# Kernel optimization log

Measured on AMD Instinct MI355X. Metric: run time of the kernel, lower is better.

The kernel has to match this reference:

```python
import jax, jax.numpy as jnp
import numpy as np


def setup_inputs() -> dict:
    key = jax.random.key(0)
    kq, kk, kv = jax.random.split(key, 3)
    B, H, S, D = 2, 16, 2048, 64
    q = jax.random.normal(kq, (B, H, S, D), dtype=jnp.float32)
    k = jax.random.normal(kk, (B, H, S, D), dtype=jnp.float32)
    v = jax.random.normal(kv, (B, H, S, D), dtype=jnp.float32)
    return {"q": q, "k": k, "v": v}


def reference(q, k, v):
    # q,k,v: [B,H,S,D]
    d_tensor = q.shape[-1]
    scale = 1.0 / jnp.sqrt(jnp.asarray(d_tensor, dtype=q.dtype))
    # score: [B,H,S,S] -- full unfused score matrix, as in the original
    score = jnp.einsum("bhsd,bhtd->bhst", q, k) * scale
    score = jax.nn.softmax(score, axis=-1)
    out = jnp.einsum("bhst,bhtd->bhsd", score, v)
    return (out, score)
```

## Files before the change

### kernel.cpp

```cpp
#include <hip/hip_runtime.h>
#include <hip/hip_bf16.h>

#define S_LEN 2048
#define D_DIM 64
#define NWAVE 4
#define NTHR  256
#define QW    32
#define QB    (QW * NWAVE)
#define NBH   32
#define CHK   128
#define NCHK  (S_LEN / CHK)
#define NE    ((size_t)NBH * S_LEN * D_DIM)

typedef __attribute__((ext_vector_type(4)))  float f32x4;
typedef __attribute__((ext_vector_type(16))) float f32x16;
typedef __attribute__((ext_vector_type(8)))  short s16x8;
typedef __attribute__((ext_vector_type(2)))  int   i32x2;

union FU { float f; unsigned int u; };
union PU { unsigned int u[4]; s16x8 v; };

__device__ __forceinline__ float bf2f(unsigned short h){
    FU x; x.u = ((unsigned int)h) << 16; return x.f;
}
__device__ __forceinline__ unsigned short f2bf(float f){
    __hip_bfloat16 h = __float2bfloat16(f);
    return __builtin_bit_cast(unsigned short, h);
}
__device__ __forceinline__ s16x8 cvt8(const float* p, float s){
    f32x4 a = *(const f32x4*)p, b = *(const f32x4*)(p + 4);
    s16x8 f;
    f[0]=(short)f2bf(a[0]*s); f[1]=(short)f2bf(a[1]*s); f[2]=(short)f2bf(a[2]*s); f[3]=(short)f2bf(a[3]*s);
    f[4]=(short)f2bf(b[0]*s); f[5]=(short)f2bf(b[1]*s); f[6]=(short)f2bf(b[2]*s); f[7]=(short)f2bf(b[3]*s);
    return f;
}

typedef __attribute__((address_space(3))) unsigned short lds_us;
typedef __attribute__((address_space(1))) const unsigned short glb_us;
__device__ __forceinline__ void gl16(const unsigned short* g, unsigned short* l){
    __builtin_amdgcn_global_load_lds((glb_us*)g, (lds_us*)l, 16, 0, 0);
}

__device__ __forceinline__ void plswap(unsigned int& a, unsigned int& b){
#if __has_builtin(__builtin_amdgcn_permlane32_swap)
    i32x2 r = __builtin_amdgcn_permlane32_swap((int)a, (int)b, false, false);
    a = (unsigned int)r[0];
    b = (unsigned int)r[1];
#else
    const int ad = ((threadIdx.x & 63) ^ 32) * 4;
    const int ax = __builtin_amdgcn_ds_bpermute(ad, (int)a);
    const int bx = __builtin_amdgcn_ds_bpermute(ad, (int)b);
    const bool hi = (threadIdx.x & 32) != 0;
    unsigned int na = hi ? (unsigned int)bx : a;
    unsigned int nb = hi ? b : (unsigned int)ax;
    a = na; b = nb;
#endif
}

__global__ __launch_bounds__(256)
void cvt_bf16_kernel(const float* __restrict__ src, unsigned short* __restrict__ dst,
                     float scale, int n8)
{
    int i = blockIdx.x * 256 + threadIdx.x;
    if (i >= n8) return;
    *(s16x8*)(dst + (size_t)i * 8) = cvt8(src + (size_t)i * 8, scale);
}

__global__ __launch_bounds__(256)
void transpose_v_kernel(const float* __restrict__ V, unsigned short* __restrict__ Vt)
{
    __shared__ float tile[64][65];
    const int bh = blockIdx.y;
    const int s0 = blockIdx.x * 64;
    const int t  = threadIdx.x;
    const int r  = t >> 2;
    const int cs = (t & 3) * 16;

    const float* src = V + ((size_t)bh * S_LEN + s0 + r) * D_DIM + cs;
    #pragma unroll
    for (int j = 0; j < 16; j += 4){
        f32x4 v = *(const f32x4*)(src + j);
        tile[r][cs + j + 0] = v[0]; tile[r][cs + j + 1] = v[1];
        tile[r][cs + j + 2] = v[2]; tile[r][cs + j + 3] = v[3];
    }
    __syncthreads();
    s16x8 o0, o1;
    #pragma unroll
    for (int j = 0; j < 8; ++j)  o0[j] = (short)f2bf(tile[cs + j][r]);
    #pragma unroll
    for (int j = 0; j < 8; ++j)  o1[j] = (short)f2bf(tile[cs + 8 + j][r]);
    unsigned short* dst = Vt + ((size_t)bh * D_DIM + r) * S_LEN + s0 + cs;
    *(s16x8*)dst       = o0;
    *(s16x8*)(dst + 8) = o1;
}

__global__ __launch_bounds__(NTHR, 2)
void sdpa_main(const unsigned short* __restrict__ Qb,
               const unsigned short* __restrict__ Kb,
               const unsigned short* __restrict__ Vt,
               float* __restrict__ Out, float* __restrict__ Score)
{
    __shared__ unsigned short kbuf[2][CHK * D_DIM];
    __shared__ unsigned short vbuf[2][D_DIM * CHK];

    const int id  = blockIdx.x;
    const int j   = id >> 3;
    const int bh  = (id & 7) * 4 + (j >> 4);
    const int qt  = j & 15;

    const int tid = threadIdx.x;
    const int w   = tid >> 6;
    const int l   = tid & 63;
    const int h   = l >> 5;
    const int q32 = l & 31;

    const unsigned short* Kbh = Kb + (size_t)bh * S_LEN * D_DIM;
    const unsigned short* Vbh = Vt + (size_t)bh * D_DIM * S_LEN;
    const int qrow = qt * QB + w * QW;

    auto stageK = [&](int c, int b){
        #pragma unroll
        for (int i = 0; i < 4; ++i){
            const int idx = i*64 + l;
            const int row = w*32 + (idx >> 3);
            const int us  = (idx & 7) ^ (row & 7);
            gl16(Kbh + ((size_t)(c*CHK + row)) * D_DIM + us*8,
                 &kbuf[b][(w*256 + i*64) * 8]);
        }
    };
    auto stageV = [&](int c, int b){
        #pragma unroll
        for (int i = 0; i < 4; ++i){
            const int idx = i*64 + l;
            const int row = w*16 + (idx >> 4);
            const int us  = (idx & 15) ^ (row & 15);
            gl16(Vbh + (size_t)row * S_LEN + c*CHK + us*8,
                 &vbuf[b][(w*256 + i*64) * 8]);
        }
    };

    s16x8 qB[4];
    {
        const unsigned short* qp = Qb + ((size_t)bh * S_LEN + qrow + q32) * D_DIM + h*8;
        #pragma unroll
        for (int s = 0; s < 4; ++s) qB[s] = *(const s16x8*)(qp + s*16);
    }

    float lsum = 0.f;
    stageK(0, 0);
    __syncthreads();
    for (int c = 0; c < NCHK; ++c){
        if (c + 1 < NCHK) stageK(c + 1, (c + 1) & 1);
        const unsigned short* kb = &kbuf[c & 1][0];
        #pragma unroll
        for (int kt = 0; kt < 4; ++kt){
            const int row = kt*32 + q32;
            f32x16 acc = {0.f,0.f,0.f,0.f,0.f,0.f,0.f,0.f,0.f,0.f,0.f,0.f,0.f,0.f,0.f,0.f};
            #pragma unroll
            for (int s = 0; s < 4; ++s){
                const int su = (2*s + h) ^ (row & 7);
                const s16x8 a = *(const s16x8*)(kb + row*D_DIM + su*8);
                acc = __builtin_amdgcn_mfma_f32_32x32x16_bf16(a, qB[s], acc, 0, 0, 0);
            }
            #pragma unroll
            for (int r = 0; r < 16; ++r)
                lsum += __expf(fminf(acc[r], 60.f));
        }
        __syncthreads();
    }
    lsum += __shfl_xor(lsum, 32, 64);
    const float invl = 1.0f / lsum;

    float invreg[16];
    #pragma unroll
    for (int r = 0; r < 16; ++r){
        const int qa = (r & 3) + 8*(r >> 2);
        invreg[r] = __shfl(invl, qa + 4*h, 64);
    }

    f32x16 oacc[2];
    oacc[0] = (f32x16){0.f,0.f,0.f,0.f,0.f,0.f,0.f,0.f,0.f,0.f,0.f,0.f,0.f,0.f,0.f,0.f};
    oacc[1] = oacc[0];

    stageK(0, 0);
    stageV(0, 0);
    __syncthreads();

    float* sbase = Score + ((size_t)bh * S_LEN + qrow + 4*h) * S_LEN + q32;

    for (int c = 0; c < NCHK; ++c){
        if (c + 1 < NCHK){ stageK(c + 1, (c + 1) & 1); stageV(c + 1, (c + 1) & 1); }
        const unsigned short* kb = &kbuf[c & 1][0];
        const unsigned short* vb = &vbuf[c & 1][0];

        #pragma unroll
        for (int kt = 0; kt < 4; ++kt){
            const int row = kt*32 + q32;
            f32x16 acc  = {0.f,0.f,0.f,0.f,0.f,0.f,0.f,0.f,0.f,0.f,0.f,0.f,0.f,0.f,0.f,0.f};
            f32x16 acc2 = acc;
            #pragma unroll
            for (int s = 0; s < 4; ++s){
                const int su = (2*s + h) ^ (row & 7);
                const s16x8 a = *(const s16x8*)(kb + row*D_DIM + su*8);
                acc  = __builtin_amdgcn_mfma_f32_32x32x16_bf16(a, qB[s], acc,  0, 0, 0);
                acc2 = __builtin_amdgcn_mfma_f32_32x32x16_bf16(qB[s], a, acc2, 0, 0, 0);
            }

            #pragma unroll
            for (int r = 0; r < 16; ++r){
                const int qa = (r & 3) + 8*(r >> 2);
                const float e = __expf(fminf(acc2[r], 60.f)) * invreg[r];
                __builtin_nontemporal_store(e, sbase + (size_t)qa * S_LEN + c*CHK + kt*32);
            }

            float e[16];
            #pragma unroll
            for (int r = 0; r < 16; ++r) e[r] = __expf(fminf(acc[r], 60.f));

            unsigned int pk[8];
            #pragma unroll
            for (int p = 0; p < 8; ++p)
                pk[p] = (unsigned int)f2bf(e[2*p]) | ((unsigned int)f2bf(e[2*p+1]) << 16);

            plswap(pk[0], pk[2]);
            plswap(pk[1], pk[3]);
            plswap(pk[4], pk[6]);
            plswap(pk[5], pk[7]);
            PU p0, p1;
            p0.u[0] = pk[0]; p0.u[1] = pk[1]; p0.u[2] = pk[2]; p0.u[3] = pk[3];
            p1.u[0] = pk[4]; p1.u[1] = pk[5]; p1.u[2] = pk[6]; p1.u[3] = pk[7];

            #pragma unroll
            for (int dt = 0; dt < 2; ++dt){
                const int d   = dt*32 + q32;
                const int su0 = (4*kt + h)     ^ (d & 15);
                const int su1 = (4*kt + 2 + h) ^ (d & 15);
                const s16x8 v0 = *(const s16x8*)(vb + d*CHK + su0*8);
                const s16x8 v1 = *(const s16x8*)(vb + d*CHK + su1*8);
                oacc[dt] = __builtin_amdgcn_mfma_f32_32x32x16_bf16(v0, p0.v, oacc[dt], 0, 0, 0);
                oacc[dt] = __builtin_amdgcn_mfma_f32_32x32x16_bf16(v1, p1.v, oacc[dt], 0, 0, 0);
            }
        }
        __syncthreads();
    }

    float* orow = Out + ((size_t)bh * S_LEN + qrow + q32) * D_DIM;
    #pragma unroll
    for (int dt = 0; dt < 2; ++dt){
        #pragma unroll
        for (int g = 0; g < 4; ++g){
            f32x4 o = { oacc[dt][4*g+0]*invl, oacc[dt][4*g+1]*invl,
                        oacc[dt][4*g+2]*invl, oacc[dt][4*g+3]*invl };
            *(f32x4*)(orow + dt*32 + 4*h + 8*g) = o;
        }
    }
}

__global__ __launch_bounds__(256)
void sdpa_naive(const float* __restrict__ Q, const float* __restrict__ K,
                const float* __restrict__ V, float* __restrict__ Out,
                float* __restrict__ Score)
{
    const int bh = blockIdx.y;
    const int qi = blockIdx.x;
    __shared__ float srow[S_LEN];
    __shared__ float qs[D_DIM];
    __shared__ float red[256];
    const int t = threadIdx.x;
    const float* qp = Q + ((size_t)bh * S_LEN + qi) * D_DIM;
    if (t < D_DIM) qs[t] = qp[t] * 0.125f;
    __syncthreads();
    float m = -1e30f;
    for (int k = t; k < S_LEN; k += 256){
        const float* kp = K + ((size_t)bh * S_LEN + k) * D_DIM;
        float s = 0.f;
        for (int d = 0; d < D_DIM; ++d) s += qs[d] * kp[d];
        srow[k] = s;
        m = fmaxf(m, s);
    }
    red[t] = m; __syncthreads();
    for (int o = 128; o; o >>= 1){ if (t < o) red[t] = fmaxf(red[t], red[t + o]); __syncthreads(); }
    m = red[0]; __syncthreads();
    float sum = 0.f;
    for (int k = t; k < S_LEN; k += 256){ float e = __expf(srow[k] - m); srow[k] = e; sum += e; }
    red[t] = sum; __syncthreads();
    for (int o = 128; o; o >>= 1){ if (t < o) red[t] += red[t + o]; __syncthreads(); }
    const float inv = 1.0f / red[0];
    float* sout = Score + ((size_t)bh * S_LEN + qi) * S_LEN;
    for (int k = t; k < S_LEN; k += 256) sout[k] = srow[k] * inv;
    if (t < D_DIM){
        float acc = 0.f;
        for (int k = 0; k < S_LEN; ++k) acc += srow[k] * V[((size_t)bh * S_LEN + k) * D_DIM + t];
        Out[((size_t)bh * S_LEN + qi) * D_DIM + t] = acc * inv;
    }
}

extern "C" void kernel_launch(void* const* d_in, const int* in_sizes, int n_in,
                              void* d_out, int out_size, void* d_ws, size_t ws_size,
                              hipStream_t stream)
{
    const float* q = (const float*)d_in[0];
    const float* k = (const float*)d_in[1];
    const float* v = (const float*)d_in[2];
    float* out   = (float*)d_out;
    float* score = out + NE;

    if (ws_size >= 3 * NE * sizeof(unsigned short)){
        unsigned short* Qb = (unsigned short*)d_ws;
        unsigned short* Kb = Qb + NE;
        unsigned short* Vt = Kb + NE;
        const int n8 = (int)(NE / 8);
        cvt_bf16_kernel<<<(n8 + 255) / 256, 256, 0, stream>>>(q, Qb, 0.125f, n8);
        cvt_bf16_kernel<<<(n8 + 255) / 256, 256, 0, stream>>>(k, Kb, 1.0f, n8);
        transpose_v_kernel<<<dim3(S_LEN / 64, NBH), 256, 0, stream>>>(v, Vt);
        sdpa_main<<<(S_LEN / QB) * NBH, NTHR, 0, stream>>>(Qb, Kb, Vt, out, score);
    } else {
        sdpa_naive<<<dim3(S_LEN, NBH), 256, 0, stream>>>(q, k, v, out, score);
    }
}
```

Before: 180.5 us.

## Split row-sum pass into separate kernel and use smaller 64-row tiles

```diff
diff --git a/kernel.cpp b/kernel.cpp
--- a/kernel.cpp
+++ b/kernel.cpp
@@ -3,14 +3,16 @@
 
 #define S_LEN 2048
 #define D_DIM 64
-#define NWAVE 4
-#define NTHR  256
-#define QW    32
-#define QB    (QW * NWAVE)
 #define NBH   32
-#define CHK   128
-#define NCHK  (S_LEN / CHK)
 #define NE    ((size_t)NBH * S_LEN * D_DIM)
+
+#define QB2   64
+#define CHK2  64
+#define NCHK2 (S_LEN / CHK2)
+
+#define QBF   128
+#define CHKF  128
+#define NCHKF (S_LEN / CHKF)
 
 typedef __attribute__((ext_vector_type(4)))  float f32x4;
 typedef __attribute__((ext_vector_type(16))) float f32x16;
@@ -94,50 +96,24 @@
     *(s16x8*)(dst + 8) = o1;
 }
 
-__global__ __launch_bounds__(NTHR, 2)
-void sdpa_main(const unsigned short* __restrict__ Qb,
-               const unsigned short* __restrict__ Kb,
-               const unsigned short* __restrict__ Vt,
-               float* __restrict__ Out, float* __restrict__ Score)
-{
-    __shared__ unsigned short kbuf[2][CHK * D_DIM];
-    __shared__ unsigned short vbuf[2][D_DIM * CHK];
-
+__global__ __launch_bounds__(128, 4)
+void pass1_lsum(const unsigned short* __restrict__ Qb,
+                const unsigned short* __restrict__ Kb,
+                float* __restrict__ invl)
+{
     const int id  = blockIdx.x;
     const int j   = id >> 3;
-    const int bh  = (id & 7) * 4 + (j >> 4);
-    const int qt  = j & 15;
+    const int bh  = (id & 7) * 4 + (j >> 5);
+    const int qt  = j & 31;
 
     const int tid = threadIdx.x;
     const int w   = tid >> 6;
     const int l   = tid & 63;
     const int h   = l >> 5;
     const int q32 = l & 31;
+    const int qrow = qt * QB2 + w * 32;
 
     const unsigned short* Kbh = Kb + (size_t)bh * S_LEN * D_DIM;
-    const unsigned short* Vbh = Vt + (size_t)bh * D_DIM * S_LEN;
-    const int qrow = qt * QB + w * QW;
-
-    auto stageK = [&](int c, int b){
-        #pragma unroll
-        for (int i = 0; i < 4; ++i){
-            const int idx = i*64 + l;
-            const int row = w*32 + (idx >> 3);
-            const int us  = (idx & 7) ^ (row & 7);
-            gl16(Kbh + ((size_t)(c*CHK + row)) * D_DIM + us*8,
-                 &kbuf[b][(w*256 + i*64) * 8]);
-        }
-    };
-    auto stageV = [&](int c, int b){
-        #pragma unroll
-        for (int i = 0; i < 4; ++i){
-            const int idx = i*64 + l;
-            const int row = w*16 + (idx >> 4);
-            const int us  = (idx & 15) ^ (row & 15);
-            gl16(Vbh + (size_t)row * S_LEN + c*CHK + us*8,
-                 &vbuf[b][(w*256 + i*64) * 8]);
-        }
-    };
 
     s16x8 qB[4];
     {
@@ -147,35 +123,82 @@
     }
 
     float lsum = 0.f;
-    stageK(0, 0);
-    __syncthreads();
-    for (int c = 0; c < NCHK; ++c){
-        if (c + 1 < NCHK) stageK(c + 1, (c + 1) & 1);
-        const unsigned short* kb = &kbuf[c & 1][0];
-        #pragma unroll
-        for (int kt = 0; kt < 4; ++kt){
-            const int row = kt*32 + q32;
-            f32x16 acc = {0.f,0.f,0.f,0.f,0.f,0.f,0.f,0.f,0.f,0.f,0.f,0.f,0.f,0.f,0.f,0.f};
-            #pragma unroll
-            for (int s = 0; s < 4; ++s){
-                const int su = (2*s + h) ^ (row & 7);
-                const s16x8 a = *(const s16x8*)(kb + row*D_DIM + su*8);
-                acc = __builtin_amdgcn_mfma_f32_32x32x16_bf16(a, qB[s], acc, 0, 0, 0);
-            }
-            #pragma unroll
-            for (int r = 0; r < 16; ++r)
-                lsum += __expf(fminf(acc[r], 60.f));
-        }
-        __syncthreads();
+    #pragma unroll 2
+    for (int kt = 0; kt < S_LEN / 32; ++kt){
+        const unsigned short* kr = Kbh + (size_t)(kt*32 + q32) * D_DIM + h*8;
+        f32x16 acc = {0.f,0.f,0.f,0.f,0.f,0.f,0.f,0.f,0.f,0.f,0.f,0.f,0.f,0.f,0.f,0.f};
+        #pragma unroll
+        for (int s = 0; s < 4; ++s){
+            const s16x8 a = *(const s16x8*)(kr + s*16);
+            acc = __builtin_amdgcn_mfma_f32_32x32x16_bf16(a, qB[s], acc, 0, 0, 0);
+        }
+        #pragma unroll
+        for (int r = 0; r < 16; ++r)
+            lsum += __expf(fminf(acc[r], 60.f));
     }
     lsum += __shfl_xor(lsum, 32, 64);
-    const float invl = 1.0f / lsum;
-
+    if (l < 32) invl[(size_t)bh * S_LEN + qrow + l] = 1.0f / lsum;
+}
+
+__global__ __launch_bounds__(128, 2)
+void sdpa_split(const unsigned short* __restrict__ Qb,
+                const unsigned short* __restrict__ Kb,
+                const unsigned short* __restrict__ Vt,
+                const float* __restrict__ invl,
+                float* __restrict__ Out, float* __restrict__ Score)
+{
+    __shared__ unsigned short kbuf[2][CHK2 * D_DIM];
+    __shared__ unsigned short vbuf[2][D_DIM * CHK2];
+
+    const int id  = blockIdx.x;
+    const int j   = id >> 3;
+    const int bh  = (id & 7) * 4 + (j >> 5);
+    const int qt  = j & 31;
+
+    const int tid = threadIdx.x;
+    const int w   = tid >> 6;
+    const int l   = tid & 63;
+    const int h   = l >> 5;
+    const int q32 = l & 31;
+    const int qrow = qt * QB2 + w * 32;
+
+    const unsigned short* Kbh = Kb + (size_t)bh * S_LEN * D_DIM;
+    const unsigned short* Vbh = Vt + (size_t)bh * D_DIM * S_LEN;
+
+    auto stageK = [&](int c, int b){
+        #pragma unroll
+        for (int i = 0; i < 4; ++i){
+            const int slot = i*128 + w*64 + l;
+            const int row  = slot >> 3;
+            const int us   = (slot & 7) ^ (row & 7);
+            gl16(Kbh + ((size_t)(c*CHK2 + row)) * D_DIM + us*8,
+                 &kbuf[b][(i*128 + w*64) * 8]);
+        }
+    };
+    auto stageV = [&](int c, int b){
+        #pragma unroll
+        for (int i = 0; i < 4; ++i){
+            const int slot = i*128 + w*64 + l;
+            const int row  = slot >> 3;
+            const int us   = (slot & 7) ^ (row & 7);
+            gl16(Vbh + (size_t)row * S_LEN + c*CHK2 + us*8,
+                 &vbuf[b][(i*128 + w*64) * 8]);
+        }
+    };
+
+    s16x8 qB[4];
+    {
+        const unsigned short* qp = Qb + ((size_t)bh * S_LEN + qrow + q32) * D_DIM + h*8;
+        #pragma unroll
+        for (int s = 0; s < 4; ++s) qB[s] = *(const s16x8*)(qp + s*16);
+    }
+
+    const float invl_lane = invl[(size_t)bh * S_LEN + qrow + q32];
     float invreg[16];
     #pragma unroll
     for (int r = 0; r < 16; ++r){
         const int qa = (r & 3) + 8*(r >> 2);
-        invreg[r] = __shfl(invl, qa + 4*h, 64);
+        invreg[r] = __shfl(invl_lane, qa + 4*h, 64);
     }
 
     f32x16 oacc[2];
@@ -188,13 +211,13 @@
 
     float* sbase = Score + ((size_t)bh * S_LEN + qrow + 4*h) * S_LEN + q32;
 
-    for (int c = 0; c < NCHK; ++c){
-        if (c + 1 < NCHK){ stageK(c + 1, (c + 1) & 1); stageV(c + 1, (c + 1) & 1); }
+    for (int c = 0; c < NCHK2; ++c){
+        if (c + 1 < NCHK2){ stageK(c + 1, (c + 1) & 1); stageV(c + 1, (c + 1) & 1); }
         const unsigned short* kb = &kbuf[c & 1][0];
         const unsigned short* vb = &vbuf[c & 1][0];
 
         #pragma unroll
-        for (int kt = 0; kt < 4; ++kt){
+        for (int kt = 0; kt < 2; ++kt){
             const int row = kt*32 + q32;
             f32x16 acc  = {0.f,0.f,0.f,0.f,0.f,0.f,0.f,0.f,0.f,0.f,0.f,0.f,0.f,0.f,0.f,0.f};
             f32x16 acc2 = acc;
@@ -210,7 +233,7 @@
             for (int r = 0; r < 16; ++r){
                 const int qa = (r & 3) + 8*(r >> 2);
                 const float e = __expf(fminf(acc2[r], 60.f)) * invreg[r];
-                __builtin_nontemporal_store(e, sbase + (size_t)qa * S_LEN + c*CHK + kt*32);
+                __builtin_nontemporal_store(e, sbase + (size_t)qa * S_LEN + c*CHK2 + kt*32);
             }
 
             float e[16];
@@ -233,10 +256,167 @@
             #pragma unroll
             for (int dt = 0; dt < 2; ++dt){
                 const int d   = dt*32 + q32;
+                const int su0 = (kt*4 + h)     ^ (d & 7);
+                const int su1 = (kt*4 + 2 + h) ^ (d & 7);
+                const s16x8 v0 = *(const s16x8*)(vb + d*CHK2 + su0*8);
+                const s16x8 v1 = *(const s16x8*)(vb + d*CHK2 + su1*8);
+                oacc[dt] = __builtin_amdgcn_mfma_f32_32x32x16_bf16(v0, p0.v, oacc[dt], 0, 0, 0);
+                oacc[dt] = __builtin_amdgcn_mfma_f32_32x32x16_bf16(v1, p1.v, oacc[dt], 0, 0, 0);
+            }
+        }
+        __syncthreads();
+    }
+
+    float* orow = Out + ((size_t)bh * S_LEN + qrow + q32) * D_DIM;
+    #pragma unroll
+    for (int dt = 0; dt < 2; ++dt){
+        #pragma unroll
+        for (int g = 0; g < 4; ++g){
+            f32x4 o = { oacc[dt][4*g+0]*invl_lane, oacc[dt][4*g+1]*invl_lane,
+                        oacc[dt][4*g+2]*invl_lane, oacc[dt][4*g+3]*invl_lane };
+            *(f32x4*)(orow + dt*32 + 4*h + 8*g) = o;
+        }
+    }
+}
+
+__global__ __launch_bounds__(256, 2)
+void sdpa_fused(const unsigned short* __restrict__ Qb,
+                const unsigned short* __restrict__ Kb,
+                const unsigned short* __restrict__ Vt,
+                float* __restrict__ Out, float* __restrict__ Score)
+{
+    __shared__ unsigned short kbuf[2][CHKF * D_DIM];
+    __shared__ unsigned short vbuf[2][D_DIM * CHKF];
+
+    const int id  = blockIdx.x;
+    const int j   = id >> 3;
+    const int bh  = (id & 7) * 4 + (j >> 4);
+    const int qt  = j & 15;
+
+    const int tid = threadIdx.x;
+    const int w   = tid >> 6;
+    const int l   = tid & 63;
+    const int h   = l >> 5;
+    const int q32 = l & 31;
+
+    const unsigned short* Kbh = Kb + (size_t)bh * S_LEN * D_DIM;
+    const unsigned short* Vbh = Vt + (size_t)bh * D_DIM * S_LEN;
+    const int qrow = qt * QBF + w * 32;
+
+    auto stageK = [&](int c, int b){
+        #pragma unroll
+        for (int i = 0; i < 4; ++i){
+            const int idx = i*64 + l;
+            const int row = w*32 + (idx >> 3);
+            const int us  = (idx & 7) ^ (row & 7);
+            gl16(Kbh + ((size_t)(c*CHKF + row)) * D_DIM + us*8,
+                 &kbuf[b][(w*256 + i*64) * 8]);
+        }
+    };
+    auto stageV = [&](int c, int b){
+        #pragma unroll
+        for (int i = 0; i < 4; ++i){
+            const int idx = i*64 + l;
+            const int row = w*16 + (idx >> 4);
+            const int us  = (idx & 15) ^ (row & 15);
+            gl16(Vbh + (size_t)row * S_LEN + c*CHKF + us*8,
+                 &vbuf[b][(w*256 + i*64) * 8]);
+        }
+    };
+
+    s16x8 qB[4];
+    {
+        const unsigned short* qp = Qb + ((size_t)bh * S_LEN + qrow + q32) * D_DIM + h*8;
+        #pragma unroll
+        for (int s = 0; s < 4; ++s) qB[s] = *(const s16x8*)(qp + s*16);
+    }
+
+    float lsum = 0.f;
+    stageK(0, 0);
+    __syncthreads();
+    for (int c = 0; c < NCHKF; ++c){
+        if (c + 1 < NCHKF) stageK(c + 1, (c + 1) & 1);
+        const unsigned short* kb = &kbuf[c & 1][0];
+        #pragma unroll
+        for (int kt = 0; kt < 4; ++kt){
+            const int row = kt*32 + q32;
+            f32x16 acc = {0.f,0.f,0.f,0.f,0.f,0.f,0.f,0.f,0.f,0.f,0.f,0.f,0.f,0.f,0.f,0.f};
+            #pragma unroll
+            for (int s = 0; s < 4; ++s){
+                const int su = (2*s + h) ^ (row & 7);
+                const s16x8 a = *(const s16x8*)(kb + row*D_DIM + su*8);
+                acc = __builtin_amdgcn_mfma_f32_32x32x16_bf16(a, qB[s], acc, 0, 0, 0);
+            }
+            #pragma unroll
+            for (int r = 0; r < 16; ++r)
+                lsum += __expf(fminf(acc[r], 60.f));
+        }
+        __syncthreads();
+    }
+    lsum += __shfl_xor(lsum, 32, 64);
+    const float invl = 1.0f / lsum;
+
+    float invreg[16];
+    #pragma unroll
+    for (int r = 0; r < 16; ++r){
+        const int qa = (r & 3) + 8*(r >> 2);
+        invreg[r] = __shfl(invl, qa + 4*h, 64);
+    }
+
+    f32x16 oacc[2];
+    oacc[0] = (f32x16){0.f,0.f,0.f,0.f,0.f,0.f,0.f,0.f,0.f,0.f,0.f,0.f,0.f,0.f,0.f,0.f};
+    oacc[1] = oacc[0];
+
+    stageK(0, 0);
+    stageV(0, 0);
+    __syncthreads();
+
+    float* sbase = Score + ((size_t)bh * S_LEN + qrow + 4*h) * S_LEN + q32;
+
+    for (int c = 0; c < NCHKF; ++c){
+        if (c + 1 < NCHKF){ stageK(c + 1, (c + 1) & 1); stageV(c + 1, (c + 1) & 1); }
+        const unsigned short* kb = &kbuf[c & 1][0];
+        const unsigned short* vb = &vbuf[c & 1][0];
+
+        #pragma unroll
+        for (int kt = 0; kt < 4; ++kt){
+            const int row = kt*32 + q32;
+            f32x16 acc  = {0.f,0.f,0.f,0.f,0.f,0.f,0.f,0.f,0.f,0.f,0.f,0.f,0.f,0.f,0.f,0.f};
+            f32x16 acc2 = acc;
+            #pragma unroll
+            for (int s = 0; s < 4; ++s){
+                const int su = (2*s + h) ^ (row & 7);
+                const s16x8 a = *(const s16x8*)(kb + row*D_DIM + su*8);
+                acc  = __builtin_amdgcn_mfma_f32_32x32x16_bf16(a, qB[s], acc,  0, 0, 0);
+                acc2 = __builtin_amdgcn_mfma_f32_32x32x16_bf16(qB[s], a, acc2, 0, 0, 0);
+            }
+            #pragma unroll
+            for (int r = 0; r < 16; ++r){
+                const int qa = (r & 3) + 8*(r >> 2);
+                const float e = __expf(fminf(acc2[r], 60.f)) * invreg[r];
+                __builtin_nontemporal_store(e, sbase + (size_t)qa * S_LEN + c*CHKF + kt*32);
+            }
+            float e[16];
+            #pragma unroll
+            for (int r = 0; r < 16; ++r) e[r] = __expf(fminf(acc[r], 60.f));
+            unsigned int pk[8];
+            #pragma unroll
+            for (int p = 0; p < 8; ++p)
+                pk[p] = (unsigned int)f2bf(e[2*p]) | ((unsigned int)f2bf(e[2*p+1]) << 16);
+            plswap(pk[0], pk[2]);
+            plswap(pk[1], pk[3]);
+            plswap(pk[4], pk[6]);
+            plswap(pk[5], pk[7]);
+            PU p0, p1;
+            p0.u[0] = pk[0]; p0.u[1] = pk[1]; p0.u[2] = pk[2]; p0.u[3] = pk[3];
+            p1.u[0] = pk[4]; p1.u[1] = pk[5]; p1.u[2] = pk[6]; p1.u[3] = pk[7];
+            #pragma unroll
+            for (int dt = 0; dt < 2; ++dt){
+                const int d   = dt*32 + q32;
                 const int su0 = (4*kt + h)     ^ (d & 15);
                 const int su1 = (4*kt + 2 + h) ^ (d & 15);
-                const s16x8 v0 = *(const s16x8*)(vb + d*CHK + su0*8);
-                const s16x8 v1 = *(const s16x8*)(vb + d*CHK + su1*8);
+                const s16x8 v0 = *(const s16x8*)(vb + d*CHKF + su0*8);
+                const s16x8 v1 = *(const s16x8*)(vb + d*CHKF + su1*8);
                 oacc[dt] = __builtin_amdgcn_mfma_f32_32x32x16_bf16(v0, p0.v, oacc[dt], 0, 0, 0);
                 oacc[dt] = __builtin_amdgcn_mfma_f32_32x32x16_bf16(v1, p1.v, oacc[dt], 0, 0, 0);
             }
@@ -305,7 +485,21 @@
     float* out   = (float*)d_out;
     float* score = out + NE;
 
-    if (ws_size >= 3 * NE * sizeof(unsigned short)){
+    const size_t need_bf16 = 3 * NE * sizeof(unsigned short);
+    const size_t need_full = need_bf16 + (size_t)NBH * S_LEN * sizeof(float);
+
+    if (ws_size >= need_full){
+        unsigned short* Qb = (unsigned short*)d_ws;
+        unsigned short* Kb = Qb + NE;
+        unsigned short* Vt = Kb + NE;
+        float* invl = (float*)(Vt + NE);
+        const int n8 = (int)(NE / 8);
+        cvt_bf16_kernel<<<(n8 + 255) / 256, 256, 0, stream>>>(q, Qb, 0.125f, n8);
+        cvt_bf16_kernel<<<(n8 + 255) / 256, 256, 0, stream>>>(k, Kb, 1.0f, n8);
+        transpose_v_kernel<<<dim3(S_LEN / 64, NBH), 256, 0, stream>>>(v, Vt);
+        pass1_lsum<<<(S_LEN / QB2) * NBH, 128, 0, stream>>>(Qb, Kb, invl);
+        sdpa_split<<<(S_LEN / QB2) * NBH, 128, 0, stream>>>(Qb, Kb, Vt, invl, out, score);
+    } else if (ws_size >= need_bf16){
         unsigned short* Qb = (unsigned short*)d_ws;
         unsigned short* Kb = Qb + NE;
         unsigned short* Vt = Kb + NE;
@@ -313,7 +507,7 @@
         cvt_bf16_kernel<<<(n8 + 255) / 256, 256, 0, stream>>>(q, Qb, 0.125f, n8);
         cvt_bf16_kernel<<<(n8 + 255) / 256, 256, 0, stream>>>(k, Kb, 1.0f, n8);
         transpose_v_kernel<<<dim3(S_LEN / 64, NBH), 256, 0, stream>>>(v, Vt);
-        sdpa_main<<<(S_LEN / QB) * NBH, NTHR, 0, stream>>>(Qb, Kb, Vt, out, score);
+        sdpa_fused<<<(S_LEN / QBF) * NBH, 256, 0, stream>>>(Qb, Kb, Vt, out, score);
     } else {
         sdpa_naive<<<dim3(S_LEN, NBH), 256, 0, stream>>>(q, k, v, out, score);
     }
```

Result: slower. 225.2 us (+24.8%).

## Drop LDS staging and load K/V fragments directly from global memory

Applied to the files above, without the earlier changes.

```diff
diff --git a/kernel.cpp b/kernel.cpp
--- a/kernel.cpp
+++ b/kernel.cpp
@@ -3,14 +3,9 @@
 
 #define S_LEN 2048
 #define D_DIM 64
-#define NWAVE 4
-#define NTHR  256
-#define QW    32
-#define QB    (QW * NWAVE)
 #define NBH   32
-#define CHK   128
-#define NCHK  (S_LEN / CHK)
 #define NE    ((size_t)NBH * S_LEN * D_DIM)
+#define NKT   (S_LEN / 32)
 
 typedef __attribute__((ext_vector_type(4)))  float f32x4;
 typedef __attribute__((ext_vector_type(16))) float f32x16;
@@ -33,12 +28,6 @@
     f[0]=(short)f2bf(a[0]*s); f[1]=(short)f2bf(a[1]*s); f[2]=(short)f2bf(a[2]*s); f[3]=(short)f2bf(a[3]*s);
     f[4]=(short)f2bf(b[0]*s); f[5]=(short)f2bf(b[1]*s); f[6]=(short)f2bf(b[2]*s); f[7]=(short)f2bf(b[3]*s);
     return f;
-}
-
-typedef __attribute__((address_space(3))) unsigned short lds_us;
-typedef __attribute__((address_space(1))) const unsigned short glb_us;
-__device__ __forceinline__ void gl16(const unsigned short* g, unsigned short* l){
-    __builtin_amdgcn_global_load_lds((glb_us*)g, (lds_us*)l, 16, 0, 0);
 }
 
 __device__ __forceinline__ void plswap(unsigned int& a, unsigned int& b){
@@ -94,15 +83,12 @@
     *(s16x8*)(dst + 8) = o1;
 }
 
-__global__ __launch_bounds__(NTHR, 2)
-void sdpa_main(const unsigned short* __restrict__ Qb,
-               const unsigned short* __restrict__ Kb,
-               const unsigned short* __restrict__ Vt,
-               float* __restrict__ Out, float* __restrict__ Score)
-{
-    __shared__ unsigned short kbuf[2][CHK * D_DIM];
-    __shared__ unsigned short vbuf[2][D_DIM * CHK];
-
+__global__ __launch_bounds__(256, 4)
+void sdpa_nolds(const unsigned short* __restrict__ Qb,
+                const unsigned short* __restrict__ Kb,
+                const unsigned short* __restrict__ Vt,
+                float* __restrict__ Out, float* __restrict__ Score)
+{
     const int id  = blockIdx.x;
     const int j   = id >> 3;
     const int bh  = (id & 7) * 4 + (j >> 4);
@@ -113,31 +99,10 @@
     const int l   = tid & 63;
     const int h   = l >> 5;
     const int q32 = l & 31;
+    const int qrow = qt * 128 + w * 32;
 
     const unsigned short* Kbh = Kb + (size_t)bh * S_LEN * D_DIM;
     const unsigned short* Vbh = Vt + (size_t)bh * D_DIM * S_LEN;
-    const int qrow = qt * QB + w * QW;
-
-    auto stageK = [&](int c, int b){
-        #pragma unroll
-        for (int i = 0; i < 4; ++i){
-            const int idx = i*64 + l;
-            const int row = w*32 + (idx >> 3);
-            const int us  = (idx & 7) ^ (row & 7);
-            gl16(Kbh + ((size_t)(c*CHK + row)) * D_DIM + us*8,
-                 &kbuf[b][(w*256 + i*64) * 8]);
-        }
-    };
-    auto stageV = [&](int c, int b){
-        #pragma unroll
-        for (int i = 0; i < 4; ++i){
-            const int idx = i*64 + l;
-            const int row = w*16 + (idx >> 4);
-            const int us  = (idx & 15) ^ (row & 15);
-            gl16(Vbh + (size_t)row * S_LEN + c*CHK + us*8,
-                 &vbuf[b][(w*256 + i*64) * 8]);
-        }
-    };
 
     s16x8 qB[4];
     {
@@ -146,27 +111,21 @@
         for (int s = 0; s < 4; ++s) qB[s] = *(const s16x8*)(qp + s*16);
     }
 
+    const unsigned short* kbase = Kbh + (size_t)q32 * D_DIM + h*8;
+
     float lsum = 0.f;
-    stageK(0, 0);
-    __syncthreads();
-    for (int c = 0; c < NCHK; ++c){
-        if (c + 1 < NCHK) stageK(c + 1, (c + 1) & 1);
-        const unsigned short* kb = &kbuf[c & 1][0];
-        #pragma unroll
-        for (int kt = 0; kt < 4; ++kt){
-            const int row = kt*32 + q32;
-            f32x16 acc = {0.f,0.f,0.f,0.f,0.f,0.f,0.f,0.f,0.f,0.f,0.f,0.f,0.f,0.f,0.f,0.f};
-            #pragma unroll
-            for (int s = 0; s < 4; ++s){
-                const int su = (2*s + h) ^ (row & 7);
-                const s16x8 a = *(const s16x8*)(kb + row*D_DIM + su*8);
-                acc = __builtin_amdgcn_mfma_f32_32x32x16_bf16(a, qB[s], acc, 0, 0, 0);
-            }
-            #pragma unroll
-            for (int r = 0; r < 16; ++r)
-                lsum += __expf(fminf(acc[r], 60.f));
-        }
-        __syncthreads();
+    #pragma unroll 2
+    for (int kt = 0; kt < NKT; ++kt){
+        const unsigned short* kr = kbase + (size_t)kt * 32 * D_DIM;
+        f32x16 acc = {0.f,0.f,0.f,0.f,0.f,0.f,0.f,0.f,0.f,0.f,0.f,0.f,0.f,0.f,0.f,0.f};
+        #pragma unroll
+        for (int s = 0; s < 4; ++s){
+            const s16x8 a = *(const s16x8*)(kr + s*16);
+            acc = __builtin_amdgcn_mfma_f32_32x32x16_bf16(a, qB[s], acc, 0, 0, 0);
+        }
+        #pragma unroll
+        for (int r = 0; r < 16; ++r)
+            lsum += __expf(fminf(acc[r], 60.f));
     }
     lsum += __shfl_xor(lsum, 32, 64);
     const float invl = 1.0f / lsum;
@@ -182,66 +141,55 @@
     oacc[0] = (f32x16){0.f,0.f,0.f,0.f,0.f,0.f,0.f,0.f,0.f,0.f,0.f,0.f,0.f,0.f,0.f,0.f};
     oacc[1] = oacc[0];
 
-    stageK(0, 0);
-    stageV(0, 0);
-    __syncthreads();
-
     float* sbase = Score + ((size_t)bh * S_LEN + qrow + 4*h) * S_LEN + q32;
 
-    for (int c = 0; c < NCHK; ++c){
-        if (c + 1 < NCHK){ stageK(c + 1, (c + 1) & 1); stageV(c + 1, (c + 1) & 1); }
-        const unsigned short* kb = &kbuf[c & 1][0];
-        const unsigned short* vb = &vbuf[c & 1][0];
-
-        #pragma unroll
-        for (int kt = 0; kt < 4; ++kt){
-            const int row = kt*32 + q32;
-            f32x16 acc  = {0.f,0.f,0.f,0.f,0.f,0.f,0.f,0.f,0.f,0.f,0.f,0.f,0.f,0.f,0.f,0.f};
-            f32x16 acc2 = acc;
-            #pragma unroll
-            for (int s = 0; s < 4; ++s){
-                const int su = (2*s + h) ^ (row & 7);
-                const s16x8 a = *(const s16x8*)(kb + row*D_DIM + su*8);
-                acc  = __builtin_amdgcn_mfma_f32_32x32x16_bf16(a, qB[s], acc,  0, 0, 0);
-                acc2 = __builtin_amdgcn_mfma_f32_32x32x16_bf16(qB[s], a, acc2, 0, 0, 0);
-            }
-
-            #pragma unroll
-            for (int r = 0; r < 16; ++r){
-                const int qa = (r & 3) + 8*(r >> 2);
-                const float e = __expf(fminf(acc2[r], 60.f)) * invreg[r];
-                __builtin_nontemporal_store(e, sbase + (size_t)qa * S_LEN + c*CHK + kt*32);
-            }
-
-            float e[16];
-            #pragma unroll
-            for (int r = 0; r < 16; ++r) e[r] = __expf(fminf(acc[r], 60.f));
-
-            unsigned int pk[8];
-            #pragma unroll
-            for (int p = 0; p < 8; ++p)
-                pk[p] = (unsigned int)f2bf(e[2*p]) | ((unsigned int)f2bf(e[2*p+1]) << 16);
-
-            plswap(pk[0], pk[2]);
-            plswap(pk[1], pk[3]);
-            plswap(pk[4], pk[6]);
-            plswap(pk[5], pk[7]);
-            PU p0, p1;
-            p0.u[0] = pk[0]; p0.u[1] = pk[1]; p0.u[2] = pk[2]; p0.u[3] = pk[3];
-            p1.u[0] = pk[4]; p1.u[1] = pk[5]; p1.u[2] = pk[6]; p1.u[3] = pk[7];
-
-            #pragma unroll
-            for (int dt = 0; dt < 2; ++dt){
-                const int d   = dt*32 + q32;
-                const int su0 = (4*kt + h)     ^ (d & 15);
-                const int su1 = (4*kt + 2 + h) ^ (d & 15);
-                const s16x8 v0 = *(const s16x8*)(vb + d*CHK + su0*8);
-                const s16x8 v1 = *(const s16x8*)(vb + d*CHK + su1*8);
-                oacc[dt] = __builtin_amdgcn_mfma_f32_32x32x16_bf16(v0, p0.v, oacc[dt], 0, 0, 0);
-                oacc[dt] = __builtin_amdgcn_mfma_f32_32x32x16_bf16(v1, p1.v, oacc[dt], 0, 0, 0);
-            }
-        }
-        __syncthreads();
+    for (int kt = 0; kt < NKT; ++kt){
+        const unsigned short* kr = kbase + (size_t)kt * 32 * D_DIM;
+        s16x8 kf[4];
+        #pragma unroll
+        for (int s = 0; s < 4; ++s) kf[s] = *(const s16x8*)(kr + s*16);
+
+        f32x16 acc2 = {0.f,0.f,0.f,0.f,0.f,0.f,0.f,0.f,0.f,0.f,0.f,0.f,0.f,0.f,0.f,0.f};
+        #pragma unroll
+        for (int s = 0; s < 4; ++s)
+            acc2 = __builtin_amdgcn_mfma_f32_32x32x16_bf16(qB[s], kf[s], acc2, 0, 0, 0);
+        #pragma unroll
+        for (int r = 0; r < 16; ++r){
+            const int qa = (r & 3) + 8*(r >> 2);
+            const float e = __expf(fminf(acc2[r], 60.f)) * invreg[r];
+            __builtin_nontemporal_store(e, sbase + (size_t)qa * S_LEN + kt*32);
+        }
+
+        f32x16 acc = {0.f,0.f,0.f,0.f,0.f,0.f,0.f,0.f,0.f,0.f,0.f,0.f,0.f,0.f,0.f,0.f};
+        #pragma unroll
+        for (int s = 0; s < 4; ++s)
+            acc = __builtin_amdgcn_mfma_f32_32x32x16_bf16(kf[s], qB[s], acc, 0, 0, 0);
+
+        float e[16];
+        #pragma unroll
+        for (int r = 0; r < 16; ++r) e[r] = __expf(fminf(acc[r], 60.f));
+
+        unsigned int pk[8];
+        #pragma unroll
+        for (int p = 0; p < 8; ++p)
+            pk[p] = (unsigned int)f2bf(e[2*p]) | ((unsigned int)f2bf(e[2*p+1]) << 16);
+
+        plswap(pk[0], pk[2]);
+        plswap(pk[1], pk[3]);
+        plswap(pk[4], pk[6]);
+        plswap(pk[5], pk[7]);
+        PU p0, p1;
+        p0.u[0] = pk[0]; p0.u[1] = pk[1]; p0.u[2] = pk[2]; p0.u[3] = pk[3];
+        p1.u[0] = pk[4]; p1.u[1] = pk[5]; p1.u[2] = pk[6]; p1.u[3] = pk[7];
+
+        #pragma unroll
+        for (int dt = 0; dt < 2; ++dt){
+            const unsigned short* vr = Vbh + (size_t)(dt*32 + q32) * S_LEN + kt*32 + h*8;
+            const s16x8 v0 = *(const s16x8*)vr;
+            const s16x8 v1 = *(const s16x8*)(vr + 16);
+            oacc[dt] = __builtin_amdgcn_mfma_f32_32x32x16_bf16(v0, p0.v, oacc[dt], 0, 0, 0);
+            oacc[dt] = __builtin_amdgcn_mfma_f32_32x32x16_bf16(v1, p1.v, oacc[dt], 0, 0, 0);
+        }
     }
 
     float* orow = Out + ((size_t)bh * S_LEN + qrow + q32) * D_DIM;
@@ -313,7 +261,7 @@
         cvt_bf16_kernel<<<(n8 + 255) / 256, 256, 0, stream>>>(q, Qb, 0.125f, n8);
         cvt_bf16_kernel<<<(n8 + 255) / 256, 256, 0, stream>>>(k, Kb, 1.0f, n8);
         transpose_v_kernel<<<dim3(S_LEN / 64, NBH), 256, 0, stream>>>(v, Vt);
-        sdpa_main<<<(S_LEN / QB) * NBH, NTHR, 0, stream>>>(Qb, Kb, Vt, out, score);
+        sdpa_nolds<<<(S_LEN / 128) * NBH, 256, 0, stream>>>(Qb, Kb, Vt, out, score);
     } else {
         sdpa_naive<<<dim3(S_LEN, NBH), 256, 0, stream>>>(q, k, v, out, score);
     }
```

New measurement: 233.0 us. +29.1%, slower.

## Shrink attention blocks to two waves and 64-key chunks, use exp2 with folded log2e

Applied to the files above, without the earlier changes.

```diff
diff --git a/kernel.cpp b/kernel.cpp
--- a/kernel.cpp
+++ b/kernel.cpp
@@ -3,14 +3,14 @@
 
 #define S_LEN 2048
 #define D_DIM 64
-#define NWAVE 4
-#define NTHR  256
-#define QW    32
-#define QB    (QW * NWAVE)
 #define NBH   32
-#define CHK   128
+#define NE    ((size_t)NBH * S_LEN * D_DIM)
+
+#define QB    64
+#define CHK   64
 #define NCHK  (S_LEN / CHK)
-#define NE    ((size_t)NBH * S_LEN * D_DIM)
+
+#define QSCALE 0.180336880146f
 
 typedef __attribute__((ext_vector_type(4)))  float f32x4;
 typedef __attribute__((ext_vector_type(16))) float f32x16;
@@ -33,6 +33,9 @@
     f[0]=(short)f2bf(a[0]*s); f[1]=(short)f2bf(a[1]*s); f[2]=(short)f2bf(a[2]*s); f[3]=(short)f2bf(a[3]*s);
     f[4]=(short)f2bf(b[0]*s); f[5]=(short)f2bf(b[1]*s); f[6]=(short)f2bf(b[2]*s); f[7]=(short)f2bf(b[3]*s);
     return f;
+}
+__device__ __forceinline__ float fexp2(float x){
+    return __builtin_amdgcn_exp2f(fminf(x, 86.0f));
 }
 
 typedef __attribute__((address_space(3))) unsigned short lds_us;
@@ -94,48 +97,48 @@
     *(s16x8*)(dst + 8) = o1;
 }
 
-__global__ __launch_bounds__(NTHR, 2)
-void sdpa_main(const unsigned short* __restrict__ Qb,
-               const unsigned short* __restrict__ Kb,
-               const unsigned short* __restrict__ Vt,
-               float* __restrict__ Out, float* __restrict__ Score)
+__global__ __launch_bounds__(128, 2)
+void sdpa_fused(const unsigned short* __restrict__ Qb,
+                const unsigned short* __restrict__ Kb,
+                const unsigned short* __restrict__ Vt,
+                float* __restrict__ Out, float* __restrict__ Score)
 {
     __shared__ unsigned short kbuf[2][CHK * D_DIM];
     __shared__ unsigned short vbuf[2][D_DIM * CHK];
 
     const int id  = blockIdx.x;
     const int j   = id >> 3;
-    const int bh  = (id & 7) * 4 + (j >> 4);
-    const int qt  = j & 15;
+    const int bh  = (id & 7) * 4 + (j >> 5);
+    const int qt  = j & 31;
 
     const int tid = threadIdx.x;
     const int w   = tid >> 6;
     const int l   = tid & 63;
     const int h   = l >> 5;
     const int q32 = l & 31;
+    const int qrow = qt * QB + w * 32;
 
     const unsigned short* Kbh = Kb + (size_t)bh * S_LEN * D_DIM;
     const unsigned short* Vbh = Vt + (size_t)bh * D_DIM * S_LEN;
-    const int qrow = qt * QB + w * QW;
 
     auto stageK = [&](int c, int b){
         #pragma unroll
         for (int i = 0; i < 4; ++i){
-            const int idx = i*64 + l;
-            const int row = w*32 + (idx >> 3);
-            const int us  = (idx & 7) ^ (row & 7);
+            const int slot = i*128 + w*64 + l;
+            const int row  = slot >> 3;
+            const int us   = (slot & 7) ^ (row & 7);
             gl16(Kbh + ((size_t)(c*CHK + row)) * D_DIM + us*8,
-                 &kbuf[b][(w*256 + i*64) * 8]);
+                 &kbuf[b][(i*128 + w*64) * 8]);
         }
     };
     auto stageV = [&](int c, int b){
         #pragma unroll
         for (int i = 0; i < 4; ++i){
-            const int idx = i*64 + l;
-            const int row = w*16 + (idx >> 4);
-            const int us  = (idx & 15) ^ (row & 15);
+            const int slot = i*128 + w*64 + l;
+            const int row  = slot >> 3;
+            const int us   = (slot & 7) ^ (row & 7);
             gl16(Vbh + (size_t)row * S_LEN + c*CHK + us*8,
-                 &vbuf[b][(w*256 + i*64) * 8]);
+                 &vbuf[b][(i*128 + w*64) * 8]);
         }
     };
 
@@ -153,7 +156,7 @@
         if (c + 1 < NCHK) stageK(c + 1, (c + 1) & 1);
         const unsigned short* kb = &kbuf[c & 1][0];
         #pragma unroll
-        for (int kt = 0; kt < 4; ++kt){
+        for (int kt = 0; kt < 2; ++kt){
             const int row = kt*32 + q32;
             f32x16 acc = {0.f,0.f,0.f,0.f,0.f,0.f,0.f,0.f,0.f,0.f,0.f,0.f,0.f,0.f,0.f,0.f};
             #pragma unroll
@@ -164,7 +167,7 @@
             }
             #pragma unroll
             for (int r = 0; r < 16; ++r)
-                lsum += __expf(fminf(acc[r], 60.f));
+                lsum += fexp2(acc[r]);
         }
         __syncthreads();
     }
@@ -194,7 +197,7 @@
         const unsigned short* vb = &vbuf[c & 1][0];
 
         #pragma unroll
-        for (int kt = 0; kt < 4; ++kt){
+        for (int kt = 0; kt < 2; ++kt){
             const int row = kt*32 + q32;
             f32x16 acc  = {0.f,0.f,0.f,0.f,0.f,0.f,0.f,0.f,0.f,0.f,0.f,0.f,0.f,0.f,0.f,0.f};
             f32x16 acc2 = acc;
@@ -209,13 +212,13 @@
             #pragma unroll
             for (int r = 0; r < 16; ++r){
                 const int qa = (r & 3) + 8*(r >> 2);
-                const float e = __expf(fminf(acc2[r], 60.f)) * invreg[r];
+                const float e = fexp2(acc2[r]) * invreg[r];
                 __builtin_nontemporal_store(e, sbase + (size_t)qa * S_LEN + c*CHK + kt*32);
             }
 
             float e[16];
             #pragma unroll
-            for (int r = 0; r < 16; ++r) e[r] = __expf(fminf(acc[r], 60.f));
+            for (int r = 0; r < 16; ++r) e[r] = fexp2(acc[r]);
 
             unsigned int pk[8];
             #pragma unroll
@@ -233,8 +236,8 @@
             #pragma unroll
             for (int dt = 0; dt < 2; ++dt){
                 const int d   = dt*32 + q32;
-                const int su0 = (4*kt + h)     ^ (d & 15);
-                const int su1 = (4*kt + 2 + h) ^ (d & 15);
+                const int su0 = (kt*4 + h)     ^ (d & 7);
+                const int su1 = (kt*4 + 2 + h) ^ (d & 7);
                 const s16x8 v0 = *(const s16x8*)(vb + d*CHK + su0*8);
                 const s16x8 v1 = *(const s16x8*)(vb + d*CHK + su1*8);
                 oacc[dt] = __builtin_amdgcn_mfma_f32_32x32x16_bf16(v0, p0.v, oacc[dt], 0, 0, 0);
@@ -310,10 +313,10 @@
         unsigned short* Kb = Qb + NE;
         unsigned short* Vt = Kb + NE;
         const int n8 = (int)(NE / 8);
-        cvt_bf16_kernel<<<(n8 + 255) / 256, 256, 0, stream>>>(q, Qb, 0.125f, n8);
+        cvt_bf16_kernel<<<(n8 + 255) / 256, 256, 0, stream>>>(q, Qb, QSCALE, n8);
         cvt_bf16_kernel<<<(n8 + 255) / 256, 256, 0, stream>>>(k, Kb, 1.0f, n8);
         transpose_v_kernel<<<dim3(S_LEN / 64, NBH), 256, 0, stream>>>(v, Vt);
-        sdpa_main<<<(S_LEN / QB) * NBH, NTHR, 0, stream>>>(Qb, Kb, Vt, out, score);
+        sdpa_fused<<<(S_LEN / QB) * NBH, 128, 0, stream>>>(Qb, Kb, Vt, out, score);
     } else {
         sdpa_naive<<<dim3(S_LEN, NBH), 256, 0, stream>>>(q, k, v, out, score);
     }
```

Result: faster. 176.9 us (-2.0%).
